# Kernel tuning notes

Measured on AMD Instinct MI355X. Metric: run time of the kernel, lower is better.

The kernel has to match this reference:

```python
import jax, jax.numpy as jnp
import numpy as np

B, S, W = 8, 256, 8
V_EXT = 32000; V_TRAIN = 32000; N_CHAR = 100; CDIM = 64; HC = 150  # char-lstm hidden per dir
D_WORD = 300; D_POS = 212; D = 512; H = 8; DK = 64; DFF = 2048; L = 6
PAD, UNK, STOP = 0, 1, 2
MAXPOS = 512


def setup_inputs() -> dict:
    key = jax.random.key(0)
    ks = jax.random.split(key, 24)
    def n(k, shape, s=0.05):
        return jax.random.normal(k, shape, jnp.float32) * s
    return {
        "word_idxs": jax.random.randint(ks[0], (B, S), 3, V_TRAIN),
        "char_idxs": jax.random.randint(ks[1], (B, S, W), 1, N_CHAR),
        "ext_emb": n(ks[2], (V_EXT, D_WORD)),
        "word_emb": n(ks[3], (V_TRAIN, D_WORD)),
        "char_emb": n(ks[4], (N_CHAR, CDIM)),
        "Wih_f": n(ks[5], (CDIM, 4 * HC), 0.1), "Whh_f": n(ks[6], (HC, 4 * HC), 0.1), "b_f": jnp.zeros((4 * HC,)),
        "Wih_b": n(ks[7], (CDIM, 4 * HC), 0.1), "Whh_b": n(ks[8], (HC, 4 * HC), 0.1), "b_b": jnp.zeros((4 * HC,)),
        "pos_emb": n(ks[9], (MAXPOS + 1, D_POS)),
        "ln0_g": jnp.ones((D,)), "ln0_b": jnp.zeros((D,)),
        "Wq": n(ks[10], (L, D, D)), "Wk": n(ks[11], (L, D, D)), "Wv": n(ks[12], (L, D, D)), "Wo": n(ks[13], (L, D, D)),
        "ln1_g": jnp.ones((L, D)), "ln1_b": jnp.zeros((L, D)),
        "W1": n(ks[14], (L, D, DFF)), "b1": jnp.zeros((L, DFF)),
        "W2": n(ks[15], (L, DFF, D)), "b2": jnp.zeros((L, D)),
        "ln2_g": jnp.ones((L, D)), "ln2_b": jnp.zeros((L, D)),
    }


def _ln(x, g, b):
    m = x.mean(-1, keepdims=True)
    v = ((x - m) ** 2).mean(-1, keepdims=True)
    return (x - m) / jnp.sqrt(v + 1e-5) * g + b


def _lstm_last(x, Wih, Whh, b, reverse):
    # x: [N, W, Din] -> final hidden [N, HC]
    N = x.shape[0]
    xs = jnp.swapaxes(x, 0, 1)
    if reverse:
        xs = xs[::-1]
    def step(carry, xt):
        h, c = carry
        g = xt @ Wih + h @ Whh + b
        i, f, gg, o = jnp.split(g, 4, axis=-1)
        c = jax.nn.sigmoid(f) * c + jax.nn.sigmoid(i) * jnp.tanh(gg)
        h = jax.nn.sigmoid(o) * jnp.tanh(c)
        return (h, c), None
    z = jnp.zeros((N, HC), x.dtype)
    (h, _), _ = jax.lax.scan(step, (z, z), xs)
    return h


def _forward(word_idxs, char_idxs, ext_emb, word_emb, char_emb, Wih_f, Whh_f, b_f,
             Wih_b, Whh_b, b_b, pos_emb, ln0_g, ln0_b, Wq, Wk, Wv, Wo,
             ln1_g, ln1_b, W1, b1, W2, b2, ln2_g, ln2_b):
    mask = word_idxs != PAD                      # [B,S] (all True for these inputs)
    sen_lens = mask.sum(1)
    pos_idxs = jnp.arange(1, S + 1)[None, :] * mask.astype(jnp.int32)
    # CharLSTM over every token's chars (mask is full, so char_idxs[mask] == flatten)
    cflat = char_emb[char_idxs.reshape(B * S, W)]
    hf = _lstm_last(cflat, Wih_f, Whh_f, b_f, False)
    hb = _lstm_last(cflat, Wih_b, Whh_b, b_b, True)
    char_vec = jnp.concatenate([hf, hb], -1).reshape(B, S, 2 * HC)
    wid = jnp.where(word_idxs >= V_TRAIN, UNK, word_idxs)
    word_vec = ext_emb[word_idxs] + word_emb[wid]
    content = word_vec + char_vec
    x = jnp.concatenate([content, pos_emb[pos_idxs]], -1)   # [B,S,D]
    x = _ln(x, ln0_g, ln0_b)
    bias = jnp.where(mask[:, None, None, :], 0.0, -1e9)
    scale = 1.0 / np.sqrt(DK).astype(np.float32)
    def layer(x, p):
        wq, wk, wv, wo, g1, be1, w1, bb1, w2, bb2, g2, be2 = p
        q = (x @ wq).reshape(B, S, H, DK)
        k = (x @ wk).reshape(B, S, H, DK)
        v = (x @ wv).reshape(B, S, H, DK)
        s = jnp.einsum('bqhd,bkhd->bhqk', q, k) * scale + bias
        a = jax.nn.softmax(s, -1)
        o = jnp.einsum('bhqk,bkhd->bqhd', a, v).reshape(B, S, D) @ wo
        x = _ln(x + o, g1, be1)
        f = jax.nn.relu(x @ w1 + bb1) @ w2 + bb2
        x = _ln(x + f, g2, be2)
        return x, None
    x, _ = jax.lax.scan(layer, x, (Wq, Wk, Wv, Wo, ln1_g, ln1_b, W1, b1, W2, b2, ln2_g, ln2_b))
    # Span features: for pair (p,q), p<q in triu order:
    #   forward  = even_ch(x[q]) - even_ch(x[p])
    #   backward = odd_ch(x[p+1]) - odd_ch(x[q+1])
    xe = x[..., 0::2]
    xo = x[..., 1::2]
    p_i, q_i = jnp.triu_indices(S - 1, k=1)      # P = (S-1)(S-2)/2 pairs
    fwd = xe[:, q_i] - xe[:, p_i]
    bwd = xo[:, p_i + 1] - xo[:, q_i + 1]
    span = jnp.concatenate([fwd, bwd], -1)        # [B,P,D]
    sentmask = (mask & (word_idxs != STOP))[:, :-1]
    valid = sentmask[:, q_i]                      # mask[b,i,j] = triu & sentmask[b,j]
    span = span * valid[..., None].astype(span.dtype)
    return span, sen_lens - 2


def reference(word_idxs, char_idxs, ext_emb, word_emb, char_emb, Wih_f, Whh_f, b_f,
              Wih_b, Whh_b, b_b, pos_emb, ln0_g, ln0_b, Wq, Wk, Wv, Wo,
              ln1_g, ln1_b, W1, b1, W2, b2, ln2_g, ln2_b):
    return _forward(word_idxs, char_idxs, ext_emb, word_emb, char_emb, Wih_f, Whh_f, b_f,
                    Wih_b, Whh_b, b_b, pos_emb, ln0_g, ln0_b, Wq, Wk, Wv, Wo,
                    ln1_g, ln1_b, W1, b1, W2, b2, ln2_g, ln2_b)
```

## Files before the change

### kernel.cpp

```cpp
#include <hip/hip_runtime.h>
#include <cstddef>
#include <cstdint>

#define BB 8
#define SS 256
#define WW 8
#define DD 512
#define HH 8
#define DKK 64
#define DFFF 2048
#define LL 6
#define NPAIR 32385
#define SPAN_TOTAL 132648960LL

typedef __attribute__((ext_vector_type(8))) short bf16x8;
typedef __attribute__((ext_vector_type(4))) float f32x4;
typedef unsigned short u16;

__device__ __forceinline__ float sigf(float x) { return 1.f / (1.f + __expf(-x)); }
__device__ __forceinline__ float tanh_fast(float x) { return 1.f - 2.f / (__expf(2.f * x) + 1.f); }

__device__ __forceinline__ void split2(float v, u16& h, u16& l) {
  unsigned u = __float_as_uint(v);
  h = (u16)(u >> 16);
  float fl = v - __uint_as_float(u & 0xffff0000u);
  l = (u16)(__float_as_uint(fl) >> 16);
}

__device__ __forceinline__ float block_sum(float v) {
  __shared__ float sb[8];
  #pragma unroll
  for (int o = 32; o > 0; o >>= 1) v += __shfl_down(v, o, 64);
  __syncthreads();
  if ((threadIdx.x & 63) == 0) sb[threadIdx.x >> 6] = v;
  __syncthreads();
  float t = 0.f;
  const int nw = blockDim.x >> 6;
  for (int i = 0; i < nw; ++i) t += sb[i];
  return t;
}

__device__ __forceinline__ float block_max(float v) {
  __shared__ float sb[8];
  #pragma unroll
  for (int o = 32; o > 0; o >>= 1) v = fmaxf(v, __shfl_down(v, o, 64));
  __syncthreads();
  if ((threadIdx.x & 63) == 0) sb[threadIdx.x >> 6] = v;
  __syncthreads();
  float t = -3.4e38f;
  const int nw = blockDim.x >> 6;
  for (int i = 0; i < nw; ++i) t = fmaxf(t, sb[i]);
  return t;
}

__global__ __launch_bounds__(256) void lstm_k(
    const int* __restrict__ char_idxs, const float* __restrict__ char_emb,
    const float* __restrict__ Wih_f, const float* __restrict__ Whh_f, const float* __restrict__ b_f,
    const float* __restrict__ Wih_b, const float* __restrict__ Whh_b, const float* __restrict__ b_b,
    float* __restrict__ hf, float* __restrict__ hb) {
  const int dir = blockIdx.y;
  const float* __restrict__ Wih = dir ? Wih_b : Wih_f;
  const float* __restrict__ Whh = dir ? Whh_b : Whh_f;
  const float* __restrict__ bv = dir ? b_b : b_f;
  float* __restrict__ dst = dir ? hb : hf;
  const int n0 = blockIdx.x * 8;
  const int tid = threadIdx.x;

  __shared__ float hs[150][8];
  __shared__ float cs[150][8];
  __shared__ float gs[8][600];
  __shared__ float xs[64][8];

  for (int i = tid; i < 1200; i += 256) { hs[i >> 3][i & 7] = 0.f; cs[i >> 3][i & 7] = 0.f; }

  const int j0 = tid, j1 = tid + 256, j2 = tid + 512;
  const bool a2 = (j2 < 600);
  const float bias0 = bv[j0], bias1 = bv[j1], bias2 = a2 ? bv[j2] : 0.f;
  __syncthreads();

  for (int st = 0; st < 8; ++st) {
    const int t = dir ? (7 - st) : st;
    for (int i = tid; i < 512; i += 256) {
      const int s = i >> 6, kk = i & 63;
      const int ci = char_idxs[(n0 + s) * 8 + t];
      xs[kk][s] = char_emb[ci * 64 + kk];
    }
    __syncthreads();

    float acc0[8], acc1[8], acc2[8];
    #pragma unroll
    for (int s = 0; s < 8; ++s) { acc0[s] = bias0; acc1[s] = bias1; acc2[s] = bias2; }

    for (int k = 0; k < 64; ++k) {
      const float w0 = Wih[k * 600 + j0];
      const float w1 = Wih[k * 600 + j1];
      const float w2 = a2 ? Wih[k * 600 + j2] : 0.f;
      const float4 xa = *(const float4*)&xs[k][0];
      const float4 xb4 = *(const float4*)&xs[k][4];
      const float xv[8] = {xa.x, xa.y, xa.z, xa.w, xb4.x, xb4.y, xb4.z, xb4.w};
      #pragma unroll
      for (int s = 0; s < 8; ++s) { acc0[s] += w0 * xv[s]; acc1[s] += w1 * xv[s]; acc2[s] += w2 * xv[s]; }
    }
    for (int k = 0; k < 150; ++k) {
      const float w0 = Whh[k * 600 + j0];
      const float w1 = Whh[k * 600 + j1];
      const float w2 = a2 ? Whh[k * 600 + j2] : 0.f;
      const float4 ha = *(const float4*)&hs[k][0];
      const float4 hb4 = *(const float4*)&hs[k][4];
      const float hv[8] = {ha.x, ha.y, ha.z, ha.w, hb4.x, hb4.y, hb4.z, hb4.w};
      #pragma unroll
      for (int s = 0; s < 8; ++s) { acc0[s] += w0 * hv[s]; acc1[s] += w1 * hv[s]; acc2[s] += w2 * hv[s]; }
    }
    #pragma unroll
    for (int s = 0; s < 8; ++s) {
      gs[s][j0] = acc0[s];
      gs[s][j1] = acc1[s];
      if (a2) gs[s][j2] = acc2[s];
    }
    __syncthreads();
    for (int i = tid; i < 1200; i += 256) {
      const int u = i >> 3, s = i & 7;
      const float ig = sigf(gs[s][u]);
      const float fg = sigf(gs[s][150 + u]);
      const float gg = tanh_fast(gs[s][300 + u]);
      const float og = sigf(gs[s][450 + u]);
      const float cc = fg * cs[u][s] + ig * gg;
      cs[u][s] = cc;
      hs[u][s] = og * tanh_fast(cc);
    }
    __syncthreads();
  }
  for (int i = tid; i < 1200; i += 256) {
    const int u = i >> 3, s = i & 7;
    dst[(size_t)(n0 + s) * 150 + u] = hs[u][s];
  }
}

__global__ __launch_bounds__(512) void embed_ln0_k(
    const int* __restrict__ word_idxs,
    const float* __restrict__ ext_emb, const float* __restrict__ word_emb,
    const float* __restrict__ hf, const float* __restrict__ hb,
    const float* __restrict__ pos_emb,
    const float* __restrict__ g, const float* __restrict__ be,
    float* __restrict__ x, u16* __restrict__ oh, u16* __restrict__ ol) {
  const int n = blockIdx.x;
  const int s = n & 255;
  const int c = threadIdx.x;
  const int w = word_idxs[n];
  const int wid = (w >= 32000) ? 1 : w;
  const int pos = (w != 0) ? (s + 1) : 0;
  float v;
  if (c < 300) {
    v = ext_emb[(size_t)w * 300 + c] + word_emb[(size_t)wid * 300 + c];
    v += (c < 150) ? hf[(size_t)n * 150 + c] : hb[(size_t)n * 150 + (c - 150)];
  } else {
    v = pos_emb[(size_t)pos * 212 + (c - 300)];
  }
  const float mean = block_sum(v) * (1.f / 512.f);
  const float d = v - mean;
  const float var = block_sum(d * d) * (1.f / 512.f);
  const float r = d * rsqrtf(var + 1e-5f) * g[c] + be[c];
  const size_t idx = (size_t)n * 512 + c;
  x[idx] = r;
  u16 h, l;
  split2(r, h, l);
  oh[idx] = h;
  ol[idx] = l;
}

__global__ __launch_bounds__(512) void ln_k(
    const float* __restrict__ inp, int nparts, long long pstride,
    const float* __restrict__ res, const float* __restrict__ bias,
    const float* __restrict__ g, const float* __restrict__ be,
    float* __restrict__ out, u16* __restrict__ oh, u16* __restrict__ ol) {
  const int n = blockIdx.x;
  const int c = threadIdx.x;
  const size_t idx = (size_t)n * 512 + c;
  float v = inp[idx];
  for (int p = 1; p < nparts; ++p) v += inp[(size_t)p * pstride + idx];
  v += res[idx];
  if (bias) v += bias[c];
  const float mean = block_sum(v) * (1.f / 512.f);
  const float d = v - mean;
  const float var = block_sum(d * d) * (1.f / 512.f);
  const float r = d * rsqrtf(var + 1e-5f) * g[c] + be[c];
  out[idx] = r;
  u16 h, l;
  split2(r, h, l);
  oh[idx] = h;
  ol[idx] = l;
}

__global__ __launch_bounds__(256) void split_k(const float* __restrict__ in,
                                               u16* __restrict__ h, u16* __restrict__ l, int n4) {
  const int i = blockIdx.x * 256 + threadIdx.x;
  if (i >= n4) return;
  const float4 v = ((const float4*)in)[i];
  ushort4 hh, ll;
  split2(v.x, hh.x, ll.x);
  split2(v.y, hh.y, ll.y);
  split2(v.z, hh.z, ll.z);
  split2(v.w, hh.w, ll.w);
  ((ushort4*)h)[i] = hh;
  ((ushort4*)l)[i] = ll;
}

__global__ __launch_bounds__(256) void wconv_k(
    const float* __restrict__ src, u16* __restrict__ dh, u16* __restrict__ dl,
    int K, int N, long long sS, long long sD) {
  const int z = blockIdx.z;
  const float* __restrict__ s = src + (size_t)z * sS;
  u16* __restrict__ oh = dh + (size_t)z * sD;
  u16* __restrict__ ol = dl + (size_t)z * sD;
  const int k0 = blockIdx.y << 6, n0 = blockIdx.x << 6;
  __shared__ float t[64][65];
  for (int i = threadIdx.x; i < 4096; i += 256) {
    const int r = i >> 6, c = i & 63;
    t[r][c] = s[(size_t)(k0 + r) * N + n0 + c];
  }
  __syncthreads();
  for (int i = threadIdx.x; i < 4096; i += 256) {
    const int nn = i >> 6, kk = i & 63;
    u16 h, l;
    split2(t[kk][nn], h, l);
    const size_t o = (size_t)(n0 + nn) * K + k0 + kk;
    oh[o] = h;
    ol[o] = l;
  }
}

template <int KSPLIT, int OMODE, int RELU>
__global__ __launch_bounds__(64) void mgemm_k(
    const u16* __restrict__ Agh, const u16* __restrict__ Agl,
    const u16* __restrict__ Bgh, const u16* __restrict__ Bgl,
    const float* __restrict__ bias,
    float* __restrict__ C, u16* __restrict__ Ch, u16* __restrict__ Cl,
    int N, int K, long long sB, long long sC) {
  const int z = blockIdx.z;
  const int bz = z / KSPLIT;
  const int ks = z - bz * KSPLIT;
  const int m0 = blockIdx.y << 6;
  const int n0 = blockIdx.x << 6;
  const int ln = threadIdx.x;

  __shared__ __align__(16) u16 SA[2][2][64][32];
  __shared__ __align__(16) u16 SB[2][2][64][32];

  const u16* __restrict__ Bh = Bgh + (size_t)bz * sB;
  const u16* __restrict__ Bl = Bgl + (size_t)bz * sB;

  const int Kc = K / KSPLIT;
  const int kbeg = ks * Kc;
  const int nsteps = Kc >> 5;

  const int srow = ln >> 2;
  const int sk = (ln & 3) << 3;

  auto stage = [&](const u16* __restrict__ src, int row0, int kt, u16* lb) {
    #pragma unroll
    for (int c = 0; c < 4; ++c) {
      const u16* g = src + (size_t)(row0 + (c << 4) + srow) * K + kt + sk;
      __builtin_amdgcn_global_load_lds(
          (__attribute__((address_space(1))) void*)g,
          (__attribute__((address_space(3))) void*)(lb + (c << 9)), 16, 0, 0);
    }
  };

  f32x4 acc[4][4];
  #pragma unroll
  for (int i = 0; i < 4; ++i)
    #pragma unroll
    for (int j = 0; j < 4; ++j)
      #pragma unroll
      for (int r = 0; r < 4; ++r) acc[i][j][r] = 0.f;

  stage(Agh, m0, kbeg, &SA[0][0][0][0]);
  stage(Agl, m0, kbeg, &SA[0][1][0][0]);
  stage(Bh, n0, kbeg, &SB[0][0][0][0]);
  stage(Bl, n0, kbeg, &SB[0][1][0][0]);

  const int lr = ln & 15;
  const int kq = (ln >> 4) << 3;

  int kt = kbeg;
  for (int t = 0; t < nsteps; ++t, kt += 32) {
    const int cb = t & 1, nb2 = cb ^ 1;
    asm volatile("s_waitcnt lgkmcnt(0)" ::: "memory");
    __builtin_amdgcn_sched_barrier(0);
    if (t + 1 < nsteps) {
      stage(Agh, m0, kt + 32, &SA[nb2][0][0][0]);
      stage(Agl, m0, kt + 32, &SA[nb2][1][0][0]);
      stage(Bh, n0, kt + 32, &SB[nb2][0][0][0]);
      stage(Bl, n0, kt + 32, &SB[nb2][1][0][0]);
      asm volatile("s_waitcnt vmcnt(16)" ::: "memory");
    } else {
      asm volatile("s_waitcnt vmcnt(0)" ::: "memory");
    }
    __builtin_amdgcn_sched_barrier(0);

    bf16x8 fa_h[4], fa_l[4], fb_h[4], fb_l[4];
    #pragma unroll
    for (int m = 0; m < 4; ++m) {
      fa_h[m] = *(const bf16x8*)&SA[cb][0][(m << 4) + lr][kq];
      fa_l[m] = *(const bf16x8*)&SA[cb][1][(m << 4) + lr][kq];
    }
    #pragma unroll
    for (int n = 0; n < 4; ++n) {
      fb_h[n] = *(const bf16x8*)&SB[cb][0][(n << 4) + lr][kq];
      fb_l[n] = *(const bf16x8*)&SB[cb][1][(n << 4) + lr][kq];
    }
    #pragma unroll
    for (int m = 0; m < 4; ++m)
      #pragma unroll
      for (int n = 0; n < 4; ++n) {
        acc[m][n] = __builtin_amdgcn_mfma_f32_16x16x32_bf16(fa_h[m], fb_h[n], acc[m][n], 0, 0, 0);
        acc[m][n] = __builtin_amdgcn_mfma_f32_16x16x32_bf16(fa_l[m], fb_h[n], acc[m][n], 0, 0, 0);
        acc[m][n] = __builtin_amdgcn_mfma_f32_16x16x32_bf16(fa_h[m], fb_l[n], acc[m][n], 0, 0, 0);
      }
  }

  const int crow = (ln >> 4) << 2;
  const int ccol = ln & 15;
  #pragma unroll
  for (int m = 0; m < 4; ++m)
    #pragma unroll
    for (int n = 0; n < 4; ++n)
      #pragma unroll
      for (int r = 0; r < 4; ++r) {
        const int row = m0 + (m << 4) + crow + r;
        const int col = n0 + (n << 4) + ccol;
        float v = acc[m][n][r];
        if (OMODE == 0) {
          if (bias) v += bias[col];
          C[(size_t)bz * sC + (size_t)row * N + col] = v;
        } else if (OMODE == 1) {
          C[(size_t)z * sC + (size_t)row * N + col] = v;
        } else {
          v += bias[col];
          if (RELU) v = fmaxf(v, 0.f);
          u16 h, l;
          split2(v, h, l);
          Ch[(size_t)row * N + col] = h;
          Cl[(size_t)row * N + col] = l;
        }
      }
}

__global__ __launch_bounds__(256) void gemm_k(
    const float* __restrict__ A, const float* __restrict__ B,
    const float* __restrict__ bias, float* __restrict__ C,
    int K, int lda, int ldb, int ldc,
    long long sA1, long long sA2, long long sB1, long long sB2,
    long long sC1, long long sC2, int bdiv, int transB, int relu) {
  __shared__ float As[16][64];
  __shared__ float Bs[16][64];
  const int bz = blockIdx.z;
  const int b1 = bz / bdiv, b2 = bz % bdiv;
  const float* __restrict__ Ab = A + b1 * sA1 + b2 * sA2;
  const float* __restrict__ Bb = B + b1 * sB1 + b2 * sB2;
  float* __restrict__ Cb = C + b1 * sC1 + b2 * sC2;
  const int n0 = blockIdx.x * 64, m0 = blockIdx.y * 64;
  const int tid = threadIdx.x;
  const int tx = tid & 15, ty = tid >> 4;
  const int lm = tid >> 2, lk4 = (tid & 3) << 2;
  const int lbk = tid >> 4, lbn4 = (tid & 15) << 2;

  float acc[4][4] = {};
  for (int kt = 0; kt < K; kt += 16) {
    const float4 av = *(const float4*)(Ab + (size_t)(m0 + lm) * lda + kt + lk4);
    float4 bv4;
    if (!transB) bv4 = *(const float4*)(Bb + (size_t)(kt + lbk) * ldb + n0 + lbn4);
    else         bv4 = *(const float4*)(Bb + (size_t)(n0 + lm) * ldb + kt + lk4);
    __syncthreads();
    As[lk4 + 0][lm] = av.x; As[lk4 + 1][lm] = av.y; As[lk4 + 2][lm] = av.z; As[lk4 + 3][lm] = av.w;
    if (!transB) { *(float4*)&Bs[lbk][lbn4] = bv4; }
    else { Bs[lk4 + 0][lm] = bv4.x; Bs[lk4 + 1][lm] = bv4.y; Bs[lk4 + 2][lm] = bv4.z; Bs[lk4 + 3][lm] = bv4.w; }
    __syncthreads();
    #pragma unroll
    for (int k = 0; k < 16; ++k) {
      const float4 a4 = *(const float4*)&As[k][ty << 2];
      const float4 b4 = *(const float4*)&Bs[k][tx << 2];
      const float ar[4] = {a4.x, a4.y, a4.z, a4.w};
      const float br[4] = {b4.x, b4.y, b4.z, b4.w};
      #pragma unroll
      for (int i = 0; i < 4; ++i)
        #pragma unroll
        for (int j = 0; j < 4; ++j)
          acc[i][j] += ar[i] * br[j];
    }
  }
  float bvv[4] = {0.f, 0.f, 0.f, 0.f};
  if (bias) {
    #pragma unroll
    for (int j = 0; j < 4; ++j) bvv[j] = bias[n0 + (tx << 2) + j];
  }
  #pragma unroll
  for (int i = 0; i < 4; ++i) {
    float vals[4];
    #pragma unroll
    for (int j = 0; j < 4; ++j) {
      float vv = acc[i][j] + bvv[j];
      if (relu) vv = fmaxf(vv, 0.f);
      vals[j] = vv;
    }
    float4 o;
    o.x = vals[0]; o.y = vals[1]; o.z = vals[2]; o.w = vals[3];
    *(float4*)(Cb + (size_t)(m0 + (ty << 2) + i) * ldc + n0 + (tx << 2)) = o;
  }
}

__global__ __launch_bounds__(256) void softmax_k(float* __restrict__ probs,
                                                 const int* __restrict__ word) {
  const int row = blockIdx.x;
  const int b = row >> 11;
  float* p = probs + (size_t)row * 256;
  const int j = threadIdx.x;
  const float s = p[j] * 0.125f + ((word[b * 256 + j] != 0) ? 0.f : -1e9f);
  const float m = block_max(s);
  const float e = __expf(s - m);
  const float t = block_sum(e);
  p[j] = e / t;
}

__device__ __forceinline__ int pair_off(int p) { return (509 * p - p * p) >> 1; }

__global__ __launch_bounds__(256) void span_k(const float* __restrict__ x,
                                              const int* __restrict__ word,
                                              float* __restrict__ out) {
  const int t = blockIdx.x;
  const int b = blockIdx.y;
  int p = (int)((509.0f - sqrtf(259081.0f - 8.0f * (float)t)) * 0.5f);
  p = max(0, min(p, 253));
  while (p < 253 && pair_off(p + 1) <= t) ++p;
  while (p > 0 && pair_off(p) > t) --p;
  const int q = p + 1 + (t - pair_off(p));
  const int w = word[b * 256 + q];
  const float valid = (w != 0 && w != 2) ? 1.f : 0.f;
  const float* xb = x + (size_t)b * 256 * 512;
  const int c = threadIdx.x;
  const float fwd = xb[(size_t)q * 512 + 2 * c] - xb[(size_t)p * 512 + 2 * c];
  const float bwd = xb[(size_t)(p + 1) * 512 + 2 * c + 1] - xb[(size_t)(q + 1) * 512 + 2 * c + 1];
  float* o = out + ((size_t)b * NPAIR + t) * 512;
  o[c] = fwd * valid;
  o[256 + c] = bwd * valid;
}

__global__ __launch_bounds__(256) void lens_k(const int* __restrict__ word,
                                              float* __restrict__ out) {
  const int b = blockIdx.x;
  const float m = (word[b * 256 + threadIdx.x] != 0) ? 1.f : 0.f;
  const float tot = block_sum(m);
  if (threadIdx.x == 0) out[b] = tot - 2.f;
}

static inline void gemm(hipStream_t st, const float* A, const float* B, const float* bias,
                        float* C, int M, int N, int K, int lda, int ldb, int ldc,
                        long long sA1, long long sA2, long long sB1, long long sB2,
                        long long sC1, long long sC2, int nb, int bdiv, int transB, int relu) {
  gemm_k<<<dim3(N / 64, M / 64, nb), 256, 0, st>>>(A, B, bias, C, K, lda, ldb, ldc,
                                                   sA1, sA2, sB1, sB2, sC1, sC2, bdiv, transB, relu);
}

extern "C" void kernel_launch(void* const* d_in, const int* in_sizes, int n_in,
                              void* d_out, int out_size, void* d_ws, size_t ws_size,
                              hipStream_t stream) {
  const int* word_idxs = (const int*)d_in[0];
  const int* char_idxs = (const int*)d_in[1];
  const float* ext_emb = (const float*)d_in[2];
  const float* word_emb = (const float*)d_in[3];
  const float* char_emb = (const float*)d_in[4];
  const float* Wih_f = (const float*)d_in[5];
  const float* Whh_f = (const float*)d_in[6];
  const float* b_f = (const float*)d_in[7];
  const float* Wih_b = (const float*)d_in[8];
  const float* Whh_b = (const float*)d_in[9];
  const float* b_b = (const float*)d_in[10];
  const float* pos_emb = (const float*)d_in[11];
  const float* ln0_g = (const float*)d_in[12];
  const float* ln0_b = (const float*)d_in[13];
  const float* Wq_a = (const float*)d_in[14];
  const float* Wk_a = (const float*)d_in[15];
  const float* Wv_a = (const float*)d_in[16];
  const float* Wo_a = (const float*)d_in[17];
  const float* ln1g = (const float*)d_in[18];
  const float* ln1b = (const float*)d_in[19];
  const float* W1_a = (const float*)d_in[20];
  const float* b1_a = (const float*)d_in[21];
  const float* W2_a = (const float*)d_in[22];
  const float* b2_a = (const float*)d_in[23];
  const float* ln2g = (const float*)d_in[24];
  const float* ln2b = (const float*)d_in[25];

  float* out = (float*)d_out;
  float* p = (float*)d_ws;
  float* hf = p;   p += 307200;
  float* hb = p;   p += 307200;
  float* x = p;    p += 1048576;
  float* qkv = p;  p += 3145728;
  float* att = p;  p += 1048576;
  float* tmp = p;  p += 4194304;
  float* prb = p;  p += 4194304;

  u16* us = (u16*)p;
  u16* xh = us;      us += 1048576;
  u16* xl = us;      us += 1048576;
  u16* ah = us;      us += 1048576;
  u16* al = us;      us += 1048576;
  u16* fhh = us;     us += 4194304;
  u16* fhl = us;     us += 4194304;
  u16* qkvT_h = us;  us += 4718592;
  u16* qkvT_l = us;  us += 4718592;
  u16* woT_h = us;   us += 1572864;
  u16* woT_l = us;   us += 1572864;
  u16* w1T_h = us;   us += 6291456;
  u16* w1T_l = us;   us += 6291456;
  u16* w2T_h = us;   us += 6291456;
  u16* w2T_l = us;   us += 6291456;

  float* qb = qkv;
  float* kb = qkv + 1048576;
  float* vb = qkv + 2097152;

  wconv_k<<<dim3(8, 8, 6), 256, 0, stream>>>(Wq_a, qkvT_h, qkvT_l, 512, 512, 262144LL, 786432LL);
  wconv_k<<<dim3(8, 8, 6), 256, 0, stream>>>(Wk_a, qkvT_h + 262144, qkvT_l + 262144, 512, 512, 262144LL, 786432LL);
  wconv_k<<<dim3(8, 8, 6), 256, 0, stream>>>(Wv_a, qkvT_h + 524288, qkvT_l + 524288, 512, 512, 262144LL, 786432LL);
  wconv_k<<<dim3(8, 8, 6), 256, 0, stream>>>(Wo_a, woT_h, woT_l, 512, 512, 262144LL, 262144LL);
  wconv_k<<<dim3(32, 8, 6), 256, 0, stream>>>(W1_a, w1T_h, w1T_l, 512, 2048, 1048576LL, 1048576LL);
  wconv_k<<<dim3(8, 32, 6), 256, 0, stream>>>(W2_a, w2T_h, w2T_l, 2048, 512, 1048576LL, 1048576LL);

  lstm_k<<<dim3(256, 2), 256, 0, stream>>>(char_idxs, char_emb, Wih_f, Whh_f, b_f,
                                           Wih_b, Whh_b, b_b, hf, hb);
  embed_ln0_k<<<2048, 512, 0, stream>>>(word_idxs, ext_emb, word_emb, hf, hb,
                                        pos_emb, ln0_g, ln0_b, x, xh, xl);

  for (int l = 0; l < LL; ++l) {
    const u16* wqh = qkvT_h + (size_t)l * 786432;
    const u16* wql = qkvT_l + (size_t)l * 786432;
    const u16* woh = woT_h + (size_t)l * 262144;
    const u16* wol = woT_l + (size_t)l * 262144;
    const u16* w1h = w1T_h + (size_t)l * 1048576;
    const u16* w1l = w1T_l + (size_t)l * 1048576;
    const u16* w2h = w2T_h + (size_t)l * 1048576;
    const u16* w2l = w2T_l + (size_t)l * 1048576;

    mgemm_k<1, 0, 0><<<dim3(8, 32, 3), 64, 0, stream>>>(
        xh, xl, wqh, wql, nullptr, qkv, nullptr, nullptr, 512, 512, 262144LL, 1048576LL);
    gemm(stream, qb, kb, nullptr, prb, 256, 256, 64, 512, 512, 256,
         131072LL, 64LL, 131072LL, 64LL, 524288LL, 65536LL, 64, 8, 1, 0);
    softmax_k<<<16384, 256, 0, stream>>>(prb, word_idxs);
    gemm(stream, prb, vb, nullptr, att, 256, 64, 256, 256, 512, 512,
         524288LL, 65536LL, 131072LL, 64LL, 131072LL, 64LL, 64, 8, 0, 0);
    split_k<<<1024, 256, 0, stream>>>(att, ah, al, 262144);
    mgemm_k<2, 1, 0><<<dim3(8, 32, 2), 64, 0, stream>>>(
        ah, al, woh, wol, nullptr, tmp, nullptr, nullptr, 512, 512, 0LL, 1048576LL);
    ln_k<<<2048, 512, 0, stream>>>(tmp, 2, 1048576LL, x, nullptr,
                                   ln1g + l * 512, ln1b + l * 512, x, xh, xl);
    mgemm_k<1, 2, 1><<<dim3(32, 32, 1), 64, 0, stream>>>(
        xh, xl, w1h, w1l, b1_a + l * 2048, nullptr, fhh, fhl, 2048, 512, 0LL, 0LL);
    mgemm_k<4, 1, 0><<<dim3(8, 32, 4), 64, 0, stream>>>(
        fhh, fhl, w2h, w2l, nullptr, tmp, nullptr, nullptr, 512, 2048, 0LL, 1048576LL);
    ln_k<<<2048, 512, 0, stream>>>(tmp, 4, 1048576LL, x, b2_a + l * 512,
                                   ln2g + l * 512, ln2b + l * 512, x, xh, xl);
  }

  span_k<<<dim3(NPAIR, 8), 256, 0, stream>>>(x, word_idxs, out);
  lens_k<<<8, 256, 0, stream>>>(word_idxs, out + (size_t)SPAN_TOTAL);
}
```

Baseline: 2.000 ms.

## Move attention QK^T and PV onto split-bf16 MFMA GEMM with fused conversions

Generalises the MFMA split-bf16 GEMM with per-batch strides and leading dimensions, then uses it for the attention score and probability-times-V products that previously ran on a scalar fp32 GEMM. The Q/K/V projections now write hi/lo bf16 pairs directly, with V stored transposed. Softmax becomes one wave per row and emits split bf16 probabilities, so the separate split pass disappears. The MFMA loop is also reordered into three passes over the accumulator tiles. The three-term bf16 split adds rounding error compared with full fp32 and more launches for Q, K and V.

```diff
diff --git a/kernel.cpp b/kernel.cpp
--- a/kernel.cpp
+++ b/kernel.cpp
@@ -37,19 +37,6 @@
   float t = 0.f;
   const int nw = blockDim.x >> 6;
   for (int i = 0; i < nw; ++i) t += sb[i];
-  return t;
-}
-
-__device__ __forceinline__ float block_max(float v) {
-  __shared__ float sb[8];
-  #pragma unroll
-  for (int o = 32; o > 0; o >>= 1) v = fmaxf(v, __shfl_down(v, o, 64));
-  __syncthreads();
-  if ((threadIdx.x & 63) == 0) sb[threadIdx.x >> 6] = v;
-  __syncthreads();
-  float t = -3.4e38f;
-  const int nw = blockDim.x >> 6;
-  for (int i = 0; i < nw; ++i) t = fmaxf(t, sb[i]);
   return t;
 }
 
@@ -191,20 +178,6 @@
   ol[idx] = l;
 }
 
-__global__ __launch_bounds__(256) void split_k(const float* __restrict__ in,
-                                               u16* __restrict__ h, u16* __restrict__ l, int n4) {
-  const int i = blockIdx.x * 256 + threadIdx.x;
-  if (i >= n4) return;
-  const float4 v = ((const float4*)in)[i];
-  ushort4 hh, ll;
-  split2(v.x, hh.x, ll.x);
-  split2(v.y, hh.y, ll.y);
-  split2(v.z, hh.z, ll.z);
-  split2(v.w, hh.w, ll.w);
-  ((ushort4*)h)[i] = hh;
-  ((ushort4*)l)[i] = ll;
-}
-
 __global__ __launch_bounds__(256) void wconv_k(
     const float* __restrict__ src, u16* __restrict__ dh, u16* __restrict__ dl,
     int K, int N, long long sS, long long sD) {
@@ -235,10 +208,13 @@
     const u16* __restrict__ Bgh, const u16* __restrict__ Bgl,
     const float* __restrict__ bias,
     float* __restrict__ C, u16* __restrict__ Ch, u16* __restrict__ Cl,
-    int N, int K, long long sB, long long sC) {
+    int K, int lda, int ldb, int ldc,
+    long long sA1, long long sA2, long long sB1, long long sB2,
+    long long sC1, long long sC2, int bdiv) {
   const int z = blockIdx.z;
   const int bz = z / KSPLIT;
   const int ks = z - bz * KSPLIT;
+  const int b1 = bz / bdiv, b2 = bz - b1 * bdiv;
   const int m0 = blockIdx.y << 6;
   const int n0 = blockIdx.x << 6;
   const int ln = threadIdx.x;
@@ -246,8 +222,10 @@
   __shared__ __align__(16) u16 SA[2][2][64][32];
   __shared__ __align__(16) u16 SB[2][2][64][32];
 
-  const u16* __restrict__ Bh = Bgh + (size_t)bz * sB;
-  const u16* __restrict__ Bl = Bgl + (size_t)bz * sB;
+  const u16* __restrict__ Ah = Agh + (size_t)b1 * sA1 + (size_t)b2 * sA2;
+  const u16* __restrict__ Al = Agl + (size_t)b1 * sA1 + (size_t)b2 * sA2;
+  const u16* __restrict__ Bh = Bgh + (size_t)b1 * sB1 + (size_t)b2 * sB2;
+  const u16* __restrict__ Bl = Bgl + (size_t)b1 * sB1 + (size_t)b2 * sB2;
 
   const int Kc = K / KSPLIT;
   const int kbeg = ks * Kc;
@@ -256,10 +234,10 @@
   const int srow = ln >> 2;
   const int sk = (ln & 3) << 3;
 
-  auto stage = [&](const u16* __restrict__ src, int row0, int kt, u16* lb) {
+  auto stage = [&](const u16* __restrict__ src, int row0, int ld, int kt, u16* lb) {
     #pragma unroll
     for (int c = 0; c < 4; ++c) {
-      const u16* g = src + (size_t)(row0 + (c << 4) + srow) * K + kt + sk;
+      const u16* g = src + (size_t)(row0 + (c << 4) + srow) * ld + kt + sk;
       __builtin_amdgcn_global_load_lds(
           (__attribute__((address_space(1))) void*)g,
           (__attribute__((address_space(3))) void*)(lb + (c << 9)), 16, 0, 0);
@@ -274,10 +252,10 @@
       #pragma unroll
       for (int r = 0; r < 4; ++r) acc[i][j][r] = 0.f;
 
-  stage(Agh, m0, kbeg, &SA[0][0][0][0]);
-  stage(Agl, m0, kbeg, &SA[0][1][0][0]);
-  stage(Bh, n0, kbeg, &SB[0][0][0][0]);
-  stage(Bl, n0, kbeg, &SB[0][1][0][0]);
+  stage(Ah, m0, lda, kbeg, &SA[0][0][0][0]);
+  stage(Al, m0, lda, kbeg, &SA[0][1][0][0]);
+  stage(Bh, n0, ldb, kbeg, &SB[0][0][0][0]);
+  stage(Bl, n0, ldb, kbeg, &SB[0][1][0][0]);
 
   const int lr = ln & 15;
   const int kq = (ln >> 4) << 3;
@@ -288,10 +266,10 @@
     asm volatile("s_waitcnt lgkmcnt(0)" ::: "memory");
     __builtin_amdgcn_sched_barrier(0);
     if (t + 1 < nsteps) {
-      stage(Agh, m0, kt + 32, &SA[nb2][0][0][0]);
-      stage(Agl, m0, kt + 32, &SA[nb2][1][0][0]);
-      stage(Bh, n0, kt + 32, &SB[nb2][0][0][0]);
-      stage(Bl, n0, kt + 32, &SB[nb2][1][0][0]);
+      stage(Ah, m0, lda, kt + 32, &SA[nb2][0][0][0]);
+      stage(Al, m0, lda, kt + 32, &SA[nb2][1][0][0]);
+      stage(Bh, n0, ldb, kt + 32, &SB[nb2][0][0][0]);
+      stage(Bl, n0, ldb, kt + 32, &SB[nb2][1][0][0]);
       asm volatile("s_waitcnt vmcnt(16)" ::: "memory");
     } else {
       asm volatile("s_waitcnt vmcnt(0)" ::: "memory");
@@ -312,15 +290,23 @@
     #pragma unroll
     for (int m = 0; m < 4; ++m)
       #pragma unroll
-      for (int n = 0; n < 4; ++n) {
+      for (int n = 0; n < 4; ++n)
         acc[m][n] = __builtin_amdgcn_mfma_f32_16x16x32_bf16(fa_h[m], fb_h[n], acc[m][n], 0, 0, 0);
+    #pragma unroll
+    for (int m = 0; m < 4; ++m)
+      #pragma unroll
+      for (int n = 0; n < 4; ++n)
         acc[m][n] = __builtin_amdgcn_mfma_f32_16x16x32_bf16(fa_l[m], fb_h[n], acc[m][n], 0, 0, 0);
+    #pragma unroll
+    for (int m = 0; m < 4; ++m)
+      #pragma unroll
+      for (int n = 0; n < 4; ++n)
         acc[m][n] = __builtin_amdgcn_mfma_f32_16x16x32_bf16(fa_h[m], fb_l[n], acc[m][n], 0, 0, 0);
-      }
   }
 
   const int crow = (ln >> 4) << 2;
   const int ccol = ln & 15;
+  const size_t cbase = (size_t)b1 * sC1 + (size_t)b2 * sC2;
   #pragma unroll
   for (int m = 0; m < 4; ++m)
     #pragma unroll
@@ -332,94 +318,58 @@
         float v = acc[m][n][r];
         if (OMODE == 0) {
           if (bias) v += bias[col];
-          C[(size_t)bz * sC + (size_t)row * N + col] = v;
+          C[cbase + (size_t)row * ldc + col] = v;
         } else if (OMODE == 1) {
-          C[(size_t)z * sC + (size_t)row * N + col] = v;
-        } else {
-          v += bias[col];
+          C[(size_t)z * sC1 + (size_t)row * ldc + col] = v;
+        } else if (OMODE == 2) {
+          if (bias) v += bias[col];
           if (RELU) v = fmaxf(v, 0.f);
           u16 h, l;
           split2(v, h, l);
-          Ch[(size_t)row * N + col] = h;
-          Cl[(size_t)row * N + col] = l;
+          Ch[cbase + (size_t)row * ldc + col] = h;
+          Cl[cbase + (size_t)row * ldc + col] = l;
+        } else {
+          u16 h, l;
+          split2(v, h, l);
+          const size_t o = ((size_t)((row >> 8) << 9) + col) * 256 + (row & 255);
+          Ch[o] = h;
+          Cl[o] = l;
         }
       }
 }
 
-__global__ __launch_bounds__(256) void gemm_k(
-    const float* __restrict__ A, const float* __restrict__ B,
-    const float* __restrict__ bias, float* __restrict__ C,
-    int K, int lda, int ldb, int ldc,
-    long long sA1, long long sA2, long long sB1, long long sB2,
-    long long sC1, long long sC2, int bdiv, int transB, int relu) {
-  __shared__ float As[16][64];
-  __shared__ float Bs[16][64];
-  const int bz = blockIdx.z;
-  const int b1 = bz / bdiv, b2 = bz % bdiv;
-  const float* __restrict__ Ab = A + b1 * sA1 + b2 * sA2;
-  const float* __restrict__ Bb = B + b1 * sB1 + b2 * sB2;
-  float* __restrict__ Cb = C + b1 * sC1 + b2 * sC2;
-  const int n0 = blockIdx.x * 64, m0 = blockIdx.y * 64;
-  const int tid = threadIdx.x;
-  const int tx = tid & 15, ty = tid >> 4;
-  const int lm = tid >> 2, lk4 = (tid & 3) << 2;
-  const int lbk = tid >> 4, lbn4 = (tid & 15) << 2;
-
-  float acc[4][4] = {};
-  for (int kt = 0; kt < K; kt += 16) {
-    const float4 av = *(const float4*)(Ab + (size_t)(m0 + lm) * lda + kt + lk4);
-    float4 bv4;
-    if (!transB) bv4 = *(const float4*)(Bb + (size_t)(kt + lbk) * ldb + n0 + lbn4);
-    else         bv4 = *(const float4*)(Bb + (size_t)(n0 + lm) * ldb + kt + lk4);
-    __syncthreads();
-    As[lk4 + 0][lm] = av.x; As[lk4 + 1][lm] = av.y; As[lk4 + 2][lm] = av.z; As[lk4 + 3][lm] = av.w;
-    if (!transB) { *(float4*)&Bs[lbk][lbn4] = bv4; }
-    else { Bs[lk4 + 0][lm] = bv4.x; Bs[lk4 + 1][lm] = bv4.y; Bs[lk4 + 2][lm] = bv4.z; Bs[lk4 + 3][lm] = bv4.w; }
-    __syncthreads();
-    #pragma unroll
-    for (int k = 0; k < 16; ++k) {
-      const float4 a4 = *(const float4*)&As[k][ty << 2];
-      const float4 b4 = *(const float4*)&Bs[k][tx << 2];
-      const float ar[4] = {a4.x, a4.y, a4.z, a4.w};
-      const float br[4] = {b4.x, b4.y, b4.z, b4.w};
-      #pragma unroll
-      for (int i = 0; i < 4; ++i)
-        #pragma unroll
-        for (int j = 0; j < 4; ++j)
-          acc[i][j] += ar[i] * br[j];
-    }
-  }
-  float bvv[4] = {0.f, 0.f, 0.f, 0.f};
-  if (bias) {
-    #pragma unroll
-    for (int j = 0; j < 4; ++j) bvv[j] = bias[n0 + (tx << 2) + j];
-  }
+__global__ __launch_bounds__(256) void softmax_k(
+    const float* __restrict__ scores, const int* __restrict__ word,
+    u16* __restrict__ ph, u16* __restrict__ pl) {
+  const int row = (blockIdx.x << 2) + (threadIdx.x >> 6);
+  const int lane = threadIdx.x & 63;
+  const int b = row >> 11;
+  const float4 s4 = ((const float4*)(scores + (size_t)row * 256))[lane];
+  const int4 w4 = ((const int4*)(word + b * 256))[lane];
+  float v[4] = {s4.x, s4.y, s4.z, s4.w};
+  const int wv[4] = {w4.x, w4.y, w4.z, w4.w};
+  float m = -3.4e38f;
   #pragma unroll
   for (int i = 0; i < 4; ++i) {
-    float vals[4];
-    #pragma unroll
-    for (int j = 0; j < 4; ++j) {
-      float vv = acc[i][j] + bvv[j];
-      if (relu) vv = fmaxf(vv, 0.f);
-      vals[j] = vv;
-    }
-    float4 o;
-    o.x = vals[0]; o.y = vals[1]; o.z = vals[2]; o.w = vals[3];
-    *(float4*)(Cb + (size_t)(m0 + (ty << 2) + i) * ldc + n0 + (tx << 2)) = o;
-  }
-}
-
-__global__ __launch_bounds__(256) void softmax_k(float* __restrict__ probs,
-                                                 const int* __restrict__ word) {
-  const int row = blockIdx.x;
-  const int b = row >> 11;
-  float* p = probs + (size_t)row * 256;
-  const int j = threadIdx.x;
-  const float s = p[j] * 0.125f + ((word[b * 256 + j] != 0) ? 0.f : -1e9f);
-  const float m = block_max(s);
-  const float e = __expf(s - m);
-  const float t = block_sum(e);
-  p[j] = e / t;
+    v[i] = v[i] * 0.125f + ((wv[i] != 0) ? 0.f : -1e9f);
+    m = fmaxf(m, v[i]);
+  }
+  #pragma unroll
+  for (int o = 32; o > 0; o >>= 1) m = fmaxf(m, __shfl_xor(m, o, 64));
+  float e[4];
+  float t = 0.f;
+  #pragma unroll
+  for (int i = 0; i < 4; ++i) { e[i] = __expf(v[i] - m); t += e[i]; }
+  #pragma unroll
+  for (int o = 32; o > 0; o >>= 1) t += __shfl_xor(t, o, 64);
+  const float rinv = 1.f / t;
+  ushort4 hh, ll;
+  split2(e[0] * rinv, hh.x, ll.x);
+  split2(e[1] * rinv, hh.y, ll.y);
+  split2(e[2] * rinv, hh.z, ll.z);
+  split2(e[3] * rinv, hh.w, ll.w);
+  ((ushort4*)(ph + (size_t)row * 256))[lane] = hh;
+  ((ushort4*)(pl + (size_t)row * 256))[lane] = ll;
 }
 
 __device__ __forceinline__ int pair_off(int p) { return (509 * p - p * p) >> 1; }
@@ -451,14 +401,6 @@
   const float m = (word[b * 256 + threadIdx.x] != 0) ? 1.f : 0.f;
   const float tot = block_sum(m);
   if (threadIdx.x == 0) out[b] = tot - 2.f;
-}
-
-static inline void gemm(hipStream_t st, const float* A, const float* B, const float* bias,
-                        float* C, int M, int N, int K, int lda, int ldb, int ldc,
-                        long long sA1, long long sA2, long long sB1, long long sB2,
-                        long long sC1, long long sC2, int nb, int bdiv, int transB, int relu) {
-  gemm_k<<<dim3(N / 64, M / 64, nb), 256, 0, st>>>(A, B, bias, C, K, lda, ldb, ldc,
-                                                   sA1, sA2, sB1, sB2, sC1, sC2, bdiv, transB, relu);
 }
 
 extern "C" void kernel_launch(void* const* d_in, const int* in_sizes, int n_in,
@@ -496,16 +438,23 @@
   float* hf = p;   p += 307200;
   float* hb = p;   p += 307200;
   float* x = p;    p += 1048576;
-  float* qkv = p;  p += 3145728;
-  float* att = p;  p += 1048576;
   float* tmp = p;  p += 4194304;
   float* prb = p;  p += 4194304;
+
+  u16* qh = (u16*)tmp;
+  u16* ql = qh + 1048576;
+  u16* kh = qh + 2097152;
+  u16* kl = qh + 3145728;
+  u16* vTh = qh + 4194304;
+  u16* vTl = qh + 5242880;
 
   u16* us = (u16*)p;
   u16* xh = us;      us += 1048576;
   u16* xl = us;      us += 1048576;
   u16* ah = us;      us += 1048576;
   u16* al = us;      us += 1048576;
+  u16* ph = us;      us += 4194304;
+  u16* pl = us;      us += 4194304;
   u16* fhh = us;     us += 4194304;
   u16* fhl = us;     us += 4194304;
   u16* qkvT_h = us;  us += 4718592;
@@ -517,10 +466,6 @@
   u16* w2T_h = us;   us += 6291456;
   u16* w2T_l = us;   us += 6291456;
 
-  float* qb = qkv;
-  float* kb = qkv + 1048576;
-  float* vb = qkv + 2097152;
-
   wconv_k<<<dim3(8, 8, 6), 256, 0, stream>>>(Wq_a, qkvT_h, qkvT_l, 512, 512, 262144LL, 786432LL);
   wconv_k<<<dim3(8, 8, 6), 256, 0, stream>>>(Wk_a, qkvT_h + 262144, qkvT_l + 262144, 512, 512, 262144LL, 786432LL);
   wconv_k<<<dim3(8, 8, 6), 256, 0, stream>>>(Wv_a, qkvT_h + 524288, qkvT_l + 524288, 512, 512, 262144LL, 786432LL);
@@ -543,22 +488,33 @@
     const u16* w2h = w2T_h + (size_t)l * 1048576;
     const u16* w2l = w2T_l + (size_t)l * 1048576;
 
-    mgemm_k<1, 0, 0><<<dim3(8, 32, 3), 64, 0, stream>>>(
-        xh, xl, wqh, wql, nullptr, qkv, nullptr, nullptr, 512, 512, 262144LL, 1048576LL);
-    gemm(stream, qb, kb, nullptr, prb, 256, 256, 64, 512, 512, 256,
-         131072LL, 64LL, 131072LL, 64LL, 524288LL, 65536LL, 64, 8, 1, 0);
-    softmax_k<<<16384, 256, 0, stream>>>(prb, word_idxs);
-    gemm(stream, prb, vb, nullptr, att, 256, 64, 256, 256, 512, 512,
-         524288LL, 65536LL, 131072LL, 64LL, 131072LL, 64LL, 64, 8, 0, 0);
-    split_k<<<1024, 256, 0, stream>>>(att, ah, al, 262144);
+    mgemm_k<1, 2, 0><<<dim3(8, 32, 1), 64, 0, stream>>>(
+        xh, xl, wqh, wql, nullptr, nullptr, qh, ql,
+        512, 512, 512, 512, 0, 0, 0, 0, 0, 0, 1);
+    mgemm_k<1, 2, 0><<<dim3(8, 32, 1), 64, 0, stream>>>(
+        xh, xl, wqh + 262144, wql + 262144, nullptr, nullptr, kh, kl,
+        512, 512, 512, 512, 0, 0, 0, 0, 0, 0, 1);
+    mgemm_k<1, 3, 0><<<dim3(8, 32, 1), 64, 0, stream>>>(
+        xh, xl, wqh + 524288, wql + 524288, nullptr, nullptr, vTh, vTl,
+        512, 512, 512, 512, 0, 0, 0, 0, 0, 0, 1);
+    mgemm_k<1, 0, 0><<<dim3(4, 4, 64), 64, 0, stream>>>(
+        qh, ql, kh, kl, nullptr, prb, nullptr, nullptr,
+        64, 512, 512, 256, 131072LL, 64LL, 131072LL, 64LL, 524288LL, 65536LL, 8);
+    softmax_k<<<4096, 256, 0, stream>>>(prb, word_idxs, ph, pl);
+    mgemm_k<1, 2, 0><<<dim3(1, 4, 64), 64, 0, stream>>>(
+        ph, pl, vTh, vTl, nullptr, nullptr, ah, al,
+        256, 256, 256, 512, 524288LL, 65536LL, 131072LL, 16384LL, 131072LL, 64LL, 8);
     mgemm_k<2, 1, 0><<<dim3(8, 32, 2), 64, 0, stream>>>(
-        ah, al, woh, wol, nullptr, tmp, nullptr, nullptr, 512, 512, 0LL, 1048576LL);
+        ah, al, woh, wol, nullptr, tmp, nullptr, nullptr,
+        512, 512, 512, 512, 0, 0, 0, 0, 1048576LL, 0, 1);
     ln_k<<<2048, 512, 0, stream>>>(tmp, 2, 1048576LL, x, nullptr,
                                    ln1g + l * 512, ln1b + l * 512, x, xh, xl);
     mgemm_k<1, 2, 1><<<dim3(32, 32, 1), 64, 0, stream>>>(
-        xh, xl, w1h, w1l, b1_a + l * 2048, nullptr, fhh, fhl, 2048, 512, 0LL, 0LL);
+        xh, xl, w1h, w1l, b1_a + l * 2048, nullptr, fhh, fhl,
+        512, 512, 512, 2048, 0, 0, 0, 0, 0, 0, 1);
     mgemm_k<4, 1, 0><<<dim3(8, 32, 4), 64, 0, stream>>>(
-        fhh, fhl, w2h, w2l, nullptr, tmp, nullptr, nullptr, 512, 2048, 0LL, 1048576LL);
+        fhh, fhl, w2h, w2l, nullptr, tmp, nullptr, nullptr,
+        2048, 2048, 2048, 512, 0, 0, 0, 0, 1048576LL, 0, 1);
     ln_k<<<2048, 512, 0, stream>>>(tmp, 4, 1048576LL, x, b2_a + l * 512,
                                    ln2g + l * 512, ln2b + l * 512, x, xh, xl);
   }
```

After: 2.088 ms. 4.4% more time.
